# Optimization experiments

Hardware: AMD Instinct MI355X
Metric: run time of the kernel (lower is better)

The kernel has to match this reference:

```python
import jax, jax.numpy as jnp
import numpy as np

EPS = 1e-5  # torch BatchNorm2d default eps (eval mode with running stats)


def bn(x, g, b, m, v):
    # x: [B,C,H,W]; per-channel affine batchnorm in inference form
    return (x - m[:, None, None]) * (g[:, None, None] / jnp.sqrt(v[:, None, None] + EPS)) + b[:, None, None]


def self_attn(x, Wq, bq, Wk, bk, Wv, bv, rel_h, rel_w):
    # x: [B,C,H,W]; Wq/Wk/Wv: [C,C] (1x1 convs); rel_h: [C,H]; rel_w: [C,W]
    B, C, H, W = x.shape
    N = H * W
    q = jnp.einsum('oc,bchw->bohw', Wq, x).reshape(B, C, N) + bq[None, :, None]
    k = jnp.einsum('oc,bchw->bohw', Wk, x).reshape(B, C, N) + bk[None, :, None]
    v = jnp.einsum('oc,bchw->bohw', Wv, x).reshape(B, C, N) + bv[None, :, None]
    energy = jnp.einsum('bcn,bcm->bnm', q, k)                      # content: Q^T K
    pos = (rel_h[:, :, None] + rel_w[:, None, :]).reshape(C, N)    # [C, H*W]
    energy = energy + jnp.einsum('bcn,cm->bnm', q, pos)            # rel-pos bias term
    attn = jax.nn.softmax(energy, axis=-1)                         # [B,N,N]
    out = jnp.einsum('bcm,bnm->bcn', v, attn)                      # V @ attn^T
    return out.reshape(B, C, H, W)


def conv3x3(x, w):
    return jax.lax.conv_general_dilated(x, w, (1, 1), 'SAME',
                                        dimension_numbers=('NCHW', 'OIHW', 'NCHW'))


def setup_inputs() -> dict:
    key = jax.random.key(0)
    B, C, H, W, NH = 32, 512, 16, 16, 5
    ks = jax.random.split(key, 32)
    f = lambda i, shape, s=1.0: jax.random.normal(ks[i], shape, jnp.float32) * s
    inp = {
        'x0': f(0, (B, C, H, W)), 'x1': f(1, (B, C, H, W)), 'x2': f(2, (B, C, H, W)),
        'x3': f(3, (B, C, H, W)), 'x': f(4, (B, C, H, W)),
        'qW': f(5, (NH, C, C), 0.02), 'qB': f(6, (NH, C), 0.02),
        'kW': f(7, (NH, C, C), 0.02), 'kB': f(8, (NH, C), 0.02),
        'vW': f(9, (NH, C, C), 0.02), 'vB': f(10, (NH, C), 0.02),
        'relH': f(11, (NH, C, H)), 'relW': f(12, (NH, C, W)),
        'msw_W': f(13, (NH - 1, NH * C), 0.02),
        'msw_g': jnp.ones((NH - 1,)), 'msw_b': jnp.zeros((NH - 1,)),
        'msw_m': jnp.zeros((NH - 1,)), 'msw_v': jnp.ones((NH - 1,)),
        'fus_W': f(14, (C, C, 3, 3), 0.02),
        'fus_g': jnp.ones((C,)), 'fus_b': jnp.zeros((C,)),
        'fus_m': jnp.zeros((C,)), 'fus_v': jnp.ones((C,)),
        'top_g': jnp.ones((C,)), 'top_b': jnp.zeros((C,)),
        'top_m': jnp.zeros((C,)), 'top_v': jnp.ones((C,)),
        'h': 16, 'w': 16,
    }
    return inp


def reference(x0, x1, x2, x3, x, qW, qB, kW, kB, vW, vB, relH, relW,
              msw_W, msw_g, msw_b, msw_m, msw_v,
              fus_W, fus_g, fus_b, fus_m, fus_v,
              top_g, top_b, top_m, top_v, h, w):
    B, C, H, W = x.shape
    xs = jnp.stack([x0, x1, x2, x3, x])                            # [5,B,C,H,W]
    outs = jax.vmap(self_attn)(xs, qW, qB, kW, kB, vW, vB, relH, relW)  # [5,B,C,H,W]
    cat = outs.transpose(1, 0, 2, 3, 4).reshape(B, 5 * C, H, W)
    weights = jax.nn.sigmoid(bn(jnp.einsum('oc,bchw->bohw', msw_W, cat),
                                msw_g, msw_b, msw_m, msw_v))        # [B,4,H,W]
    x_ms = (weights[:, 0:1] * outs[0] + weights[:, 1:2] * outs[1]
            + weights[:, 2:3] * outs[2] + weights[:, 3:4] * outs[3] + outs[4])
    x_ms = jax.nn.relu(bn(conv3x3(x_ms, fus_W), fus_g, fus_b, fus_m, fus_v))
    out = jax.nn.relu(bn(x_ms + x, top_g, top_b, top_m, top_v))
    return out
```

## Files before the change

### kernel.cpp

```cpp
#include <hip/hip_runtime.h>
#include <cstdint>

using bf16x8  = __attribute__((ext_vector_type(8))) __bf16;
using f32x4   = __attribute__((ext_vector_type(4))) float;
using ushort8 = __attribute__((ext_vector_type(8))) unsigned short;

#define EPSN 1e-5f

__device__ __forceinline__ void gld16(const void* g, void* l) {
  __builtin_amdgcn_global_load_lds((const __attribute__((address_space(1))) void*)g,
                                   (__attribute__((address_space(3))) void*)l, 16, 0, 0);
}

__device__ __forceinline__ ushort f2bf(float f) {
  __bf16 h = (__bf16)f;
  return __builtin_bit_cast(unsigned short, h);
}
__device__ __forceinline__ float bf2f(ushort u) {
  union { uint32_t u; float f; } v; v.u = ((uint32_t)u) << 16; return v.f;
}

__global__ __launch_bounds__(256) void k_pre(const float* __restrict__ x0,
                                             const float* __restrict__ x1,
                                             const float* __restrict__ x2,
                                             const float* __restrict__ x3,
                                             const float* __restrict__ x4,
                                             const float* __restrict__ qW,
                                             const float* __restrict__ kW,
                                             const float* __restrict__ vW,
                                             const float* __restrict__ relH,
                                             const float* __restrict__ relW,
                                             const float* __restrict__ fg,
                                             const float* __restrict__ fb,
                                             const float* __restrict__ fm,
                                             const float* __restrict__ fv,
                                             const float* __restrict__ tg,
                                             const float* __restrict__ tb,
                                             const float* __restrict__ tm,
                                             const float* __restrict__ tv,
                                             ushort* __restrict__ xT,
                                             ushort* __restrict__ Wb,
                                             ushort* __restrict__ posb,
                                             float4* __restrict__ bnp) {
  __shared__ float tile[64][65];
  int bid = blockIdx.x;
  const int t = threadIdx.x;
  if (bid < 5120) {
    const int nt4 = bid & 3;  bid >>= 2;
    const int ct  = bid & 7;  bid >>= 3;
    const int b   = bid & 31; bid >>= 5;
    const int ix  = bid;
    const float* xs = ix == 0 ? x0 : ix == 1 ? x1 : ix == 2 ? x2 : ix == 3 ? x3 : x4;
    const float* src = xs + ((size_t)b * 512 + ct * 64) * 256 + nt4 * 64;
    const int col4 = (t & 15) * 4, r0 = t >> 4;
#pragma unroll
    for (int p = 0; p < 4; ++p) {
      int row = p * 16 + r0;
      float4 v = *(const float4*)(src + (size_t)row * 256 + col4);
      tile[row][col4 + 0] = v.x; tile[row][col4 + 1] = v.y;
      tile[row][col4 + 2] = v.z; tile[row][col4 + 3] = v.w;
    }
    __syncthreads();
    ushort* dst = xT + ((size_t)(ix * 32 + b) * 256 + nt4 * 64) * 512 + ct * 64;
    const int c8 = (t & 7) * 8, n0 = t >> 3;
#pragma unroll
    for (int p = 0; p < 2; ++p) {
      int nrow = p * 32 + n0;
      ushort8 o;
#pragma unroll
      for (int e = 0; e < 8; ++e) o[e] = f2bf(tile[c8 + e][nrow]);
      *(ushort8*)(dst + (size_t)nrow * 512 + c8) = o;
    }
  } else if (bid < 8960) {
    int idx = (bid - 5120) * 256 + t;
    int gi = idx * 4;
    int sel = gi / 1310720;
    int off = gi - sel * 1310720;
    const float* src = sel == 0 ? qW : (sel == 1 ? kW : vW);
    float4 vv = *(const float4*)(src + off);
    int h = off / 262144, rest = off - h * 262144;
    ushort4 o;
    o.x = f2bf(vv.x); o.y = f2bf(vv.y); o.z = f2bf(vv.z); o.w = f2bf(vv.w);
    *(ushort4*)(Wb + (size_t)(h * 3 + sel) * 262144 + rest) = o;
  } else if (bid < 9280) {
    int idx8 = (bid - 8960) * 256 + t;
    int e0 = idx8 * 8;
    int c0 = e0 & 511, m = (e0 >> 9) & 255, h = e0 >> 17;
    ushort8 o;
#pragma unroll
    for (int e = 0; e < 8; ++e) {
      int c = c0 + e;
      o[e] = f2bf(relH[((size_t)h * 512 + c) * 16 + (m >> 4)] +
                  relW[((size_t)h * 512 + c) * 16 + (m & 15)]);
    }
    *(ushort8*)(posb + e0) = o;
  } else {
    int o = (bid - 9280) * 256 + t;
    float sf = fg[o] * rsqrtf(fv[o] + EPSN);
    float c1 = fb[o] - fm[o] * sf;
    float st = tg[o] * rsqrtf(tv[o] + EPSN);
    float c2 = tb[o] - tm[o] * st;
    bnp[o] = make_float4(sf, c1, st, c2);
  }
}

__global__ __launch_bounds__(512, 4) void k_qkv3(const ushort* __restrict__ Wb,
                                                 const ushort* __restrict__ xT,
                                                 const ushort* __restrict__ posb,
                                                 const float* __restrict__ qB,
                                                 const float* __restrict__ kB,
                                                 const float* __restrict__ vB,
                                                 ushort* __restrict__ qT,
                                                 ushort* __restrict__ kpT,
                                                 ushort* __restrict__ vv) {
  extern __shared__ ushort ls[];
  const int t = threadIdx.x, lane = t & 63;
  const int w = t >> 6, wm = w >> 2, wn = w & 3, g = lane >> 4, l = lane & 15;
  int bid = blockIdx.x;
  bid = (bid & 7) * 240 + (bid >> 3);
  const int h = bid / 384;
  const int r = bid % 384;

  const ushort* Ag;
  const ushort* Bg;
  const bool partA = r < 256;
  int pt = 0, nt = 0, mt = 0, ntv = 0;
  if (partA) {
    pt = r >> 2; nt = r & 3;
    Ag = xT + ((size_t)h * 8192 + pt * 128) * 512;
    Bg = Wb + ((size_t)(h * 3 + (nt >> 1)) * 512 + (nt & 1) * 256) * 512;
  } else {
    const int r2 = r - 256;
    mt = r2 >> 5; ntv = r2 & 31;
    Ag = Wb + ((size_t)(h * 3 + 2) * 512 + mt * 128) * 512;
    Bg = xT + ((size_t)h * 8192 + ntv * 256) * 512;
  }

  f32x4 acc[4][4];
#pragma unroll
  for (int i = 0; i < 4; ++i)
#pragma unroll
    for (int j = 0; j < 4; ++j) acc[i][j] = f32x4{0.f, 0.f, 0.f, 0.f};

#define QKV_STAGE(tt, slot)                                                    \
  {                                                                            \
    const int kb_ = (tt) * 32;                                                 \
    ushort* sa_ = ls + (slot) * 4096;                                          \
    ushort* sb_ = ls + 12288 + (slot) * 8192;                                  \
    {                                                                          \
      int q_ = t;                                                              \
      int row_ = q_ >> 2, s4_ = q_ & 3;                                        \
      int src_ = s4_ ^ ((row_ ^ (row_ >> 2)) & 3);                             \
      gld16(Ag + (size_t)row_ * 512 + kb_ + src_ * 8, sa_ + q_ * 8);           \
    }                                                                          \
    _Pragma("unroll")                                                          \
    for (int p_ = 0; p_ < 2; ++p_) {                                           \
      int q_ = p_ * 512 + t;                                                   \
      int row_ = q_ >> 2, s4_ = q_ & 3;                                        \
      int src_ = s4_ ^ ((row_ ^ (row_ >> 2)) & 3);                             \
      gld16(Bg + (size_t)row_ * 512 + kb_ + src_ * 8, sb_ + q_ * 8);           \
    }                                                                          \
  }

#define QKV_COMPUTE(slot)                                                      \
  {                                                                            \
    ushort* sa_ = ls + (slot) * 4096;                                          \
    ushort* sb_ = ls + 12288 + (slot) * 8192;                                  \
    bf16x8 af[4], bfv[4];                                                      \
    _Pragma("unroll")                                                          \
    for (int j_ = 0; j_ < 4; ++j_) {                                           \
      int rb_ = wn * 64 + j_ * 16 + l;                                         \
      int sb2_ = g ^ ((rb_ ^ (rb_ >> 2)) & 3);                                 \
      bfv[j_] = *(const bf16x8*)(sb_ + rb_ * 32 + sb2_ * 8);                   \
    }                                                                          \
    _Pragma("unroll")                                                          \
    for (int i_ = 0; i_ < 4; ++i_) {                                           \
      int ra_ = wm * 64 + i_ * 16 + l;                                         \
      int sa2_ = g ^ ((ra_ ^ (ra_ >> 2)) & 3);                                 \
      af[i_] = *(const bf16x8*)(sa_ + ra_ * 32 + sa2_ * 8);                    \
    }                                                                          \
    asm volatile("s_waitcnt lgkmcnt(0)" ::: "memory");                         \
    __builtin_amdgcn_sched_barrier(0);                                         \
    __builtin_amdgcn_s_setprio(1);                                             \
    _Pragma("unroll")                                                          \
    for (int i_ = 0; i_ < 4; ++i_)                                             \
      _Pragma("unroll")                                                        \
      for (int j_ = 0; j_ < 4; ++j_)                                           \
        acc[i_][j_] = __builtin_amdgcn_mfma_f32_16x16x32_bf16(af[i_], bfv[j_], \
                                                              acc[i_][j_], 0, 0, 0); \
    __builtin_amdgcn_s_setprio(0);                                             \
  }

  QKV_STAGE(0, 0);
  QKV_STAGE(1, 1);
  for (int tt = 0; tt < 16; ++tt) {
    __builtin_amdgcn_s_barrier();
    if (tt < 14) { QKV_STAGE(tt + 2, (tt + 2) % 3); }
    __builtin_amdgcn_sched_barrier(0);
    if (tt < 14)       asm volatile("s_waitcnt vmcnt(6)" ::: "memory");
    else if (tt == 14) asm volatile("s_waitcnt vmcnt(3)" ::: "memory");
    else               asm volatile("s_waitcnt vmcnt(0)" ::: "memory");
    __builtin_amdgcn_s_barrier();
    __builtin_amdgcn_sched_barrier(0);
    QKV_COMPUTE(tt % 3);
  }
  __syncthreads();

  ushort(*Cs)[260] = (ushort(*)[260])ls;
  if (partA) {
    const bool isq = nt < 2;
    const float* bias = (isq ? qB : kB) + (size_t)h * 512 + (nt & 1) * 256;
    ushort* dst = isq ? qT : kpT;
    float bj[4];
#pragma unroll
    for (int j = 0; j < 4; ++j) bj[j] = bias[wn * 64 + j * 16 + l];
#pragma unroll
    for (int R = 0; R < 2; ++R) {
      if (wm == R) {
#pragma unroll
        for (int i = 0; i < 4; ++i)
#pragma unroll
          for (int j = 0; j < 4; ++j)
#pragma unroll
            for (int rr = 0; rr < 4; ++rr)
              Cs[i * 16 + g * 4 + rr][wn * 64 + j * 16 + l] = f2bf(acc[i][j][rr] + bj[j]);
      }
      __syncthreads();
#pragma unroll
      for (int it = 0; it < 4; ++it) {
        int lin = it * 512 + t;
        int row = lin >> 5, cc8 = (lin & 31) * 8;
        int pglob = pt * 128 + R * 64 + row;
        ushort8 cv = *(const ushort8*)&Cs[row][cc8];
        if (!isq) {
          ushort8 pv = *(const ushort8*)(posb + ((size_t)h * 256 + (pglob & 255)) * 512 +
                                         (nt & 1) * 256 + cc8);
#pragma unroll
          for (int e = 0; e < 8; ++e) cv[e] = f2bf(bf2f(cv[e]) + bf2f(pv[e]));
        }
        *(ushort8*)(dst + ((size_t)h * 8192 + pglob) * 512 + (nt & 1) * 256 + cc8) = cv;
      }
      if (R == 0) __syncthreads();
    }
  } else {
    const float* bias = vB + (size_t)h * 512 + mt * 128;
#pragma unroll
    for (int R = 0; R < 2; ++R) {
      if (wm == R) {
#pragma unroll
        for (int i = 0; i < 4; ++i) {
          float4 b4 = *(const float4*)(bias + R * 64 + i * 16 + g * 4);
#pragma unroll
          for (int j = 0; j < 4; ++j)
#pragma unroll
            for (int rr = 0; rr < 4; ++rr)
              Cs[i * 16 + g * 4 + rr][wn * 64 + j * 16 + l] =
                  f2bf(acc[i][j][rr] + ((const float*)&b4)[rr]);
        }
      }
      __syncthreads();
#pragma unroll
      for (int it = 0; it < 4; ++it) {
        int lin = it * 512 + t;
        int row = lin >> 5, cc8 = (lin & 31) * 8;
        int og = mt * 128 + R * 64 + row;
        ushort8 cv = *(const ushort8*)&Cs[row][cc8];
        *(ushort8*)(vv + (((size_t)(h * 32 + ntv)) * 512 + og) * 256 + cc8) = cv;
      }
      if (R == 0) __syncthreads();
    }
  }
#undef QKV_STAGE
#undef QKV_COMPUTE
}

__global__ __launch_bounds__(256) void k_attn(const ushort* __restrict__ qT,
                                              const ushort* __restrict__ kpT,
                                              const float* __restrict__ fusW,
                                              ushort* __restrict__ attn,
                                              ushort* __restrict__ Wconv) {
  __shared__ ushort sm[20480];
  __shared__ float red[4][64];
  __shared__ float comb[64];
  int bid = blockIdx.x;
  const int t = threadIdx.x;
  if (bid >= 640) {
    int p = (bid - 640) * 256 + t;
    const float* src = fusW + (size_t)p * 9;
    float vv[9];
#pragma unroll
    for (int s = 0; s < 9; ++s) vv[s] = src[s];
#pragma unroll
    for (int s = 0; s < 9; ++s) Wconv[(size_t)s * 262144 + p] = f2bf(vv[s]);
    return;
  }
  bid = (bid & 7) * 80 + (bid >> 3);
  const int rt = bid & 3;
  const int hb = bid >> 2;
  ushort* As = sm;
  ushort* Bs = sm + 4096;
  const ushort* Ag = qT + ((size_t)hb * 256 + rt * 64) * 512;
  const ushort* Bg = kpT + (size_t)hb * 256 * 512;
  const int lane = t & 63, w = t >> 6, g = lane >> 4, l = lane & 15;

  f32x4 acc[4][4];
#pragma unroll
  for (int i = 0; i < 4; ++i)
#pragma unroll
    for (int j = 0; j < 4; ++j) acc[i][j] = f32x4{0.f, 0.f, 0.f, 0.f};

  for (int kt = 0; kt < 8; ++kt) {
    const int kbase = kt * 64;
#pragma unroll
    for (int p = 0; p < 2; ++p) {
      int q = p * 256 + t;
      int row = q >> 3, slot = q & 7, srcs = slot ^ (row & 7);
      gld16(Ag + (size_t)row * 512 + kbase + srcs * 8, As + (p * 256 + w * 64) * 8);
    }
#pragma unroll
    for (int p = 0; p < 8; ++p) {
      int q = p * 256 + t;
      int row = q >> 3, slot = q & 7, srcs = slot ^ (row & 7);
      gld16(Bg + (size_t)row * 512 + kbase + srcs * 8, Bs + (p * 256 + w * 64) * 8);
    }
    __syncthreads();
#pragma unroll
    for (int kk = 0; kk < 2; ++kk) {
      bf16x8 af[4], bfv[4];
#pragma unroll
      for (int i = 0; i < 4; ++i) {
        int ra = i * 16 + l;
        int sa = (kk * 4 + g) ^ (ra & 7);
        af[i] = *(const bf16x8*)(As + ra * 64 + sa * 8);
        int rb = w * 64 + i * 16 + l;
        int sb = (kk * 4 + g) ^ (rb & 7);
        bfv[i] = *(const bf16x8*)(Bs + rb * 64 + sb * 8);
      }
#pragma unroll
      for (int i = 0; i < 4; ++i)
#pragma unroll
        for (int j = 0; j < 4; ++j)
          acc[i][j] = __builtin_amdgcn_mfma_f32_16x16x32_bf16(af[i], bfv[j], acc[i][j], 0, 0, 0);
    }
    __syncthreads();
  }

#pragma unroll
  for (int i = 0; i < 4; ++i)
#pragma unroll
    for (int rr = 0; rr < 4; ++rr) {
      float v = fmaxf(fmaxf(acc[i][0][rr], acc[i][1][rr]), fmaxf(acc[i][2][rr], acc[i][3][rr]));
#pragma unroll
      for (int m = 1; m < 16; m <<= 1) v = fmaxf(v, __shfl_xor(v, m));
      if (l == 0) red[w][i * 16 + g * 4 + rr] = v;
    }
  __syncthreads();
  if (t < 64) comb[t] = fmaxf(fmaxf(red[0][t], red[1][t]), fmaxf(red[2][t], red[3][t]));
  __syncthreads();
#pragma unroll
  for (int i = 0; i < 4; ++i)
#pragma unroll
    for (int rr = 0; rr < 4; ++rr) {
      float mx = comb[i * 16 + g * 4 + rr];
      float s = 0.f;
#pragma unroll
      for (int j = 0; j < 4; ++j) {
        float e = expf(acc[i][j][rr] - mx);
        acc[i][j][rr] = e;
        s += e;
      }
#pragma unroll
      for (int m = 1; m < 16; m <<= 1) s += __shfl_xor(s, m);
      if (l == 0) red[w][i * 16 + g * 4 + rr] = s;
    }
  __syncthreads();
  if (t < 64) comb[t] = red[0][t] + red[1][t] + red[2][t] + red[3][t];
  __syncthreads();
  ushort(*P)[260] = (ushort(*)[260])sm;
#pragma unroll
  for (int i = 0; i < 4; ++i)
#pragma unroll
    for (int rr = 0; rr < 4; ++rr) {
      int row = i * 16 + g * 4 + rr;
      float inv = 1.f / comb[row];
#pragma unroll
      for (int j = 0; j < 4; ++j)
        P[row][w * 64 + j * 16 + l] = f2bf(acc[i][j][rr] * inv);
    }
  __syncthreads();
  ushort* Arow = attn + (size_t)hb * 65536 + (size_t)rt * 16384;
#pragma unroll
  for (int it = 0; it < 8; ++it) {
    int lin = it * 256 + t;
    int row = lin >> 5, c8 = (lin & 31) * 8;
    ushort8 cv = *(const ushort8*)&P[row][c8];
    *(ushort8*)(Arow + (size_t)row * 256 + c8) = cv;
  }
}

__global__ __launch_bounds__(256, 4) void k_pv(const ushort* __restrict__ attn,
                                               const ushort* __restrict__ vv,
                                               ushort* __restrict__ OT) {
  __shared__ ushort pls[24576];
  const int t = threadIdx.x, lane = t & 63, w = t >> 6;
  const int wr = w >> 1, wc = w & 1, g = lane >> 4, l = lane & 15;
  int bid = blockIdx.x;
  bid = (bid & 7) * 160 + (bid >> 3);
  const int nt = bid & 3; bid >>= 2;
  const int mt = bid & 1; bid >>= 1;
  const size_t hb = (size_t)bid;
  const ushort* Ag = attn + (hb * 256 + mt * 128) * 256;
  const ushort* Bg = vv + (hb * 512 + nt * 128) * 256;

  f32x4 acc[4][4];
#pragma unroll
  for (int i = 0; i < 4; ++i)
#pragma unroll
    for (int j = 0; j < 4; ++j) acc[i][j] = f32x4{0.f, 0.f, 0.f, 0.f};

#define PV_STAGE(tt, slot)                                                     \
  {                                                                            \
    const int kb_ = (tt) * 32;                                                 \
    ushort* sa_ = pls + (slot) * 4096;                                         \
    ushort* sb_ = pls + 12288 + (slot) * 4096;                                 \
    _Pragma("unroll")                                                          \
    for (int p_ = 0; p_ < 2; ++p_) {                                           \
      int q_ = p_ * 256 + t;                                                   \
      int row_ = q_ >> 2, s4_ = q_ & 3;                                        \
      int src_ = s4_ ^ ((row_ ^ (row_ >> 2)) & 3);                             \
      gld16(Ag + (size_t)row_ * 256 + kb_ + src_ * 8, sa_ + q_ * 8);           \
      gld16(Bg + (size_t)row_ * 256 + kb_ + src_ * 8, sb_ + q_ * 8);           \
    }                                                                          \
  }

#define PV_COMPUTE(slot)                                                       \
  {                                                                            \
    ushort* sa_ = pls + (slot) * 4096;                                         \
    ushort* sb_ = pls + 12288 + (slot) * 4096;                                 \
    bf16x8 af[4], bfv[4];                                                      \
    _Pragma("unroll")                                                          \
    for (int i_ = 0; i_ < 4; ++i_) {                                           \
      int ra_ = wr * 64 + i_ * 16 + l;                                         \
      int sa2_ = g ^ ((ra_ ^ (ra_ >> 2)) & 3);                                 \
      af[i_] = *(const bf16x8*)(sa_ + ra_ * 32 + sa2_ * 8);                    \
      int rb_ = wc * 64 + i_ * 16 + l;                                         \
      int sb2_ = g ^ ((rb_ ^ (rb_ >> 2)) & 3);                                 \
      bfv[i_] = *(const bf16x8*)(sb_ + rb_ * 32 + sb2_ * 8);                   \
    }                                                                          \
    asm volatile("s_waitcnt lgkmcnt(0)" ::: "memory");                         \
    __builtin_amdgcn_sched_barrier(0);                                         \
    __builtin_amdgcn_s_setprio(1);                                             \
    _Pragma("unroll")                                                          \
    for (int i_ = 0; i_ < 4; ++i_)                                             \
      _Pragma("unroll")                                                        \
      for (int j_ = 0; j_ < 4; ++j_)                                           \
        acc[i_][j_] = __builtin_amdgcn_mfma_f32_16x16x32_bf16(af[i_], bfv[j_], \
                                                              acc[i_][j_], 0, 0, 0); \
    __builtin_amdgcn_s_setprio(0);                                             \
  }

  PV_STAGE(0, 0);
  PV_STAGE(1, 1);
  for (int tt = 0; tt < 8; ++tt) {
    __builtin_amdgcn_s_barrier();
    if (tt < 6) { PV_STAGE(tt + 2, (tt + 2) % 3); }
    __builtin_amdgcn_sched_barrier(0);
    if (tt < 6)       asm volatile("s_waitcnt vmcnt(8)" ::: "memory");
    else if (tt == 6) asm volatile("s_waitcnt vmcnt(4)" ::: "memory");
    else              asm volatile("s_waitcnt vmcnt(0)" ::: "memory");
    __builtin_amdgcn_s_barrier();
    __builtin_amdgcn_sched_barrier(0);
    PV_COMPUTE(tt % 3);
  }
  __syncthreads();

  ushort(*Cs)[148] = (ushort(*)[148])pls;
#pragma unroll
  for (int i = 0; i < 4; ++i)
#pragma unroll
    for (int j = 0; j < 4; ++j)
#pragma unroll
      for (int rr = 0; rr < 4; ++rr)
        Cs[wr * 64 + i * 16 + g * 4 + rr][wc * 64 + j * 16 + l] = f2bf(acc[i][j][rr]);
  __syncthreads();
#pragma unroll
  for (int it = 0; it < 8; ++it) {
    int lin = it * 256 + t;
    int row = lin >> 4, cc = (lin & 15) * 8;
    ushort8 cv = *(const ushort8*)&Cs[row][cc];
    *(ushort8*)(OT + (hb * 256 + mt * 128 + row) * 512 + nt * 128 + cc) = cv;
  }
#undef PV_STAGE
#undef PV_COMPUTE
}

__global__ __launch_bounds__(256) void k_weights(const ushort* __restrict__ OT,
                                                 const float* __restrict__ mswW,
                                                 const float* __restrict__ mg,
                                                 const float* __restrict__ mb,
                                                 const float* __restrict__ mm,
                                                 const float* __restrict__ mv,
                                                 ushort* __restrict__ xmsT) {
  __shared__ float msw[10240];
  const int t = threadIdx.x, lane = t & 63, w = t >> 6;
#pragma unroll
  for (int it = 0; it < 10; ++it) {
    int idx = it * 1024 + t * 4;
    *(float4*)(msw + idx) = *(const float4*)(mswW + idx);
  }
  __syncthreads();
  const size_t pix = (size_t)blockIdx.x * 4 + w;
  float o[5][2][4];
#pragma unroll
  for (int h = 0; h < 5; ++h)
#pragma unroll
    for (int hf = 0; hf < 2; ++hf) {
      ushort4 v = *(const ushort4*)(OT + ((size_t)h * 8192 + pix) * 512 + hf * 256 + lane * 4);
      o[h][hf][0] = bf2f(v.x); o[h][hf][1] = bf2f(v.y);
      o[h][hf][2] = bf2f(v.z); o[h][hf][3] = bf2f(v.w);
    }
  float a[4] = {0.f, 0.f, 0.f, 0.f};
#pragma unroll
  for (int j = 0; j < 4; ++j)
#pragma unroll
    for (int h = 0; h < 5; ++h)
#pragma unroll
      for (int hf = 0; hf < 2; ++hf) {
        float4 m4 = *(const float4*)(msw + j * 2560 + h * 512 + hf * 256 + lane * 4);
        a[j] += m4.x * o[h][hf][0] + m4.y * o[h][hf][1] +
                m4.z * o[h][hf][2] + m4.w * o[h][hf][3];
      }
#pragma unroll
  for (int m = 1; m < 64; m <<= 1) {
    a[0] += __shfl_xor(a[0], m); a[1] += __shfl_xor(a[1], m);
    a[2] += __shfl_xor(a[2], m); a[3] += __shfl_xor(a[3], m);
  }
  float wj[4];
#pragma unroll
  for (int j = 0; j < 4; ++j) {
    float val = (a[j] - mm[j]) * (mg[j] * rsqrtf(mv[j] + EPSN)) + mb[j];
    wj[j] = 1.f / (1.f + expf(-val));
  }
#pragma unroll
  for (int hf = 0; hf < 2; ++hf) {
    float r0 = wj[0] * o[0][hf][0] + wj[1] * o[1][hf][0] + wj[2] * o[2][hf][0] + wj[3] * o[3][hf][0] + o[4][hf][0];
    float r1 = wj[0] * o[0][hf][1] + wj[1] * o[1][hf][1] + wj[2] * o[2][hf][1] + wj[3] * o[3][hf][1] + o[4][hf][1];
    float r2 = wj[0] * o[0][hf][2] + wj[1] * o[1][hf][2] + wj[2] * o[2][hf][2] + wj[3] * o[3][hf][2] + o[4][hf][2];
    float r3 = wj[0] * o[0][hf][3] + wj[1] * o[1][hf][3] + wj[2] * o[2][hf][3] + wj[3] * o[3][hf][3] + o[4][hf][3];
    ushort4 pk; pk.x = f2bf(r0); pk.y = f2bf(r1); pk.z = f2bf(r2); pk.w = f2bf(r3);
    *(ushort4*)(xmsT + pix * 512 + hf * 256 + lane * 4) = pk;
  }
}

__global__ __launch_bounds__(256) void k_conv(const ushort* __restrict__ Wconv,
                                              const ushort* __restrict__ xmsT,
                                              const float* __restrict__ x,
                                              const float4* __restrict__ bnp,
                                              float* __restrict__ out) {
  __shared__ ushort As3[3 * 4096];
  __shared__ ushort xp[180 * 76];
  int bid = blockIdx.x;
  bid = (bid & 7) * 64 + (bid >> 3);
  const int ntl = bid & 1; bid >>= 1;
  const int mt = bid & 7;  bid >>= 3;
  const int bb = bid;
  const int y0 = ntl * 8;
  const int t = threadIdx.x, lane = t & 63;
  const int w = t >> 6, wm = w >> 1, wn = w & 1, g = lane >> 4, l = lane & 15;
  f32x4 acc[2][4];
#pragma unroll
  for (int i = 0; i < 2; ++i)
#pragma unroll
    for (int j = 0; j < 4; ++j) acc[i][j] = f32x4{0.f, 0.f, 0.f, 0.f};

  for (int cb = 0; cb < 8; ++cb) {
    __syncthreads();
    for (int u = t; u < 1440; u += 256) {
      int slot = u & 7;
      int xpi = (u >> 3) % 18;
      int rl = u / 144;
      int yg = y0 - 1 + rl, xg = xpi - 1;
      uint4 val = make_uint4(0, 0, 0, 0);
      if (yg >= 0 && yg < 16 && (unsigned)xg < 16u)
        val = *(const uint4*)(xmsT + ((size_t)bb * 256 + yg * 16 + xg) * 512 + cb * 64 + slot * 8);
      *(uint4*)(xp + (rl * 18 + xpi) * 76 + slot * 8) = val;
    }
    for (int dy = 0; dy < 3; ++dy) {
#pragma unroll
      for (int dx = 0; dx < 3; ++dx)
#pragma unroll
        for (int p = 0; p < 2; ++p) {
          int q = p * 256 + t;
          int row = q >> 3, slot = q & 7, srcs = slot ^ (row & 7);
          gld16(Wconv + ((size_t)(dy * 3 + dx) * 512 + mt * 64 + row) * 512 + cb * 64 + srcs * 8,
                As3 + dx * 4096 + q * 8);
        }
      __syncthreads();
#pragma unroll
      for (int dx = 0; dx < 3; ++dx)
#pragma unroll
        for (int kk = 0; kk < 2; ++kk) {
          bf16x8 af[2], bfv[4];
#pragma unroll
          for (int j = 0; j < 4; ++j) {
            int nl = wn * 64 + j * 16 + l;
            int pp = ((nl >> 4) + dy) * 18 + (nl & 15) + dx;
            bfv[j] = *(const bf16x8*)(xp + pp * 76 + (kk * 4 + g) * 8);
          }
#pragma unroll
          for (int i = 0; i < 2; ++i) {
            int ra = wm * 32 + i * 16 + l;
            int sa = (kk * 4 + g) ^ (ra & 7);
            af[i] = *(const bf16x8*)(As3 + dx * 4096 + ra * 64 + sa * 8);
          }
#pragma unroll
          for (int i = 0; i < 2; ++i)
#pragma unroll
            for (int j = 0; j < 4; ++j)
              acc[i][j] = __builtin_amdgcn_mfma_f32_16x16x32_bf16(af[i], bfv[j], acc[i][j], 0, 0, 0);
        }
      __syncthreads();
    }
  }
  const int o0 = mt * 64 + wm * 32;
#pragma unroll
  for (int i = 0; i < 2; ++i)
#pragma unroll
    for (int rr = 0; rr < 4; ++rr) {
      int o = o0 + i * 16 + g * 4 + rr;
      float4 p4 = bnp[o];
#pragma unroll
      for (int j = 0; j < 4; ++j) {
        int n = ntl * 128 + wn * 64 + j * 16 + l;
        size_t idx = ((size_t)bb * 512 + o) * 256 + n;
        float z = fmaxf(acc[i][j][rr] * p4.x + p4.y, 0.f);
        out[idx] = fmaxf((z + x[idx]) * p4.z + p4.w, 0.f);
      }
    }
}

extern "C" void kernel_launch(void* const* d_in, const int* in_sizes, int n_in,
                              void* d_out, int out_size, void* d_ws, size_t ws_size,
                              hipStream_t stream) {
  const float* x0   = (const float*)d_in[0];
  const float* x1   = (const float*)d_in[1];
  const float* x2   = (const float*)d_in[2];
  const float* x3   = (const float*)d_in[3];
  const float* x4   = (const float*)d_in[4];
  const float* qW   = (const float*)d_in[5];
  const float* qB   = (const float*)d_in[6];
  const float* kW   = (const float*)d_in[7];
  const float* kB   = (const float*)d_in[8];
  const float* vW   = (const float*)d_in[9];
  const float* vB   = (const float*)d_in[10];
  const float* relH = (const float*)d_in[11];
  const float* relW = (const float*)d_in[12];
  const float* mswW = (const float*)d_in[13];
  const float* msg  = (const float*)d_in[14];
  const float* msb  = (const float*)d_in[15];
  const float* msm  = (const float*)d_in[16];
  const float* msv  = (const float*)d_in[17];
  const float* fusW = (const float*)d_in[18];
  const float* fg   = (const float*)d_in[19];
  const float* fb   = (const float*)d_in[20];
  const float* fm   = (const float*)d_in[21];
  const float* fv   = (const float*)d_in[22];
  const float* tg   = (const float*)d_in[23];
  const float* tb   = (const float*)d_in[24];
  const float* tm   = (const float*)d_in[25];
  const float* tv   = (const float*)d_in[26];

  if (ws_size < 180355072ull) return;
  char* ws = (char*)d_ws;
  ushort* xT    = (ushort*)(ws + 0);
  ushort* attn  = (ushort*)(ws + 0);
  ushort* Wconv = (ushort*)(ws + 20971520);
  ushort* qT    = (ushort*)(ws + 41943040);
  ushort* xmsT  = (ushort*)(ws + 41943040);
  ushort* kpT   = (ushort*)(ws + 83886080);
  ushort* OT    = (ushort*)(ws + 83886080);
  ushort* vv    = (ushort*)(ws + 125829120);
  ushort* Wb    = (ushort*)(ws + 167772160);
  ushort* posb  = (ushort*)(ws + 175636480);
  float4* bnp   = (float4*)(ws + 176947200);

  hipFuncSetAttribute((const void*)k_qkv3,
                      hipFuncAttributeMaxDynamicSharedMemorySize, 73728);

  k_pre    <<<9282, 256, 0, stream>>>(x0, x1, x2, x3, x4, qW, kW, vW, relH, relW,
                                      fg, fb, fm, fv, tg, tb, tm, tv,
                                      xT, Wb, posb, (float4*)bnp);
  k_qkv3   <<<1920, 512, 73728, stream>>>(Wb, xT, posb, qB, kB, vB, qT, kpT, vv);
  k_attn   <<<1664, 256, 0, stream>>>(qT, kpT, fusW, attn, Wconv);
  k_pv     <<<1280, 256, 0, stream>>>(attn, vv, OT);
  k_weights<<<2048, 256, 0, stream>>>(OT, mswW, msg, msb, msm, msv, xmsT);
  k_conv   <<<512,  256, 0, stream>>>(Wconv, xmsT, x4, bnp, (float*)d_out);
}
```

Measured before the change: 246.4 us.

## Triple-buffer attention QK GEMM loads and batch four pixels per weights wave

The QK^T stage of the attention kernel now uses a three-slot LDS ring with a K-step of 32. Loads for two future tiles stay in flight while MFMAs run on the current one, with explicit vmcnt waits, raw barriers and setprio around the MFMA block. A new XOR swizzle keeps LDS reads free of bank conflicts. Separately, the mixing-weights kernel now handles four pixels per wave, so each 40KB msw weight copy into LDS is amortized over 16 pixels and the grid drops to 512 blocks. This trades more LDS use and hand-tuned wait counts (fragile if load counts change) for better load/compute overlap.

Result: slower. 275.1 us (+11.7%).

```diff
diff --git a/kernel.cpp b/kernel.cpp
--- a/kernel.cpp
+++ b/kernel.cpp
@@ -279,7 +279,7 @@
                                               const float* __restrict__ fusW,
                                               ushort* __restrict__ attn,
                                               ushort* __restrict__ Wconv) {
-  __shared__ ushort sm[20480];
+  __shared__ ushort sm[30720];
   __shared__ float red[4][64];
   __shared__ float comb[64];
   int bid = blockIdx.x;
@@ -297,8 +297,6 @@
   bid = (bid & 7) * 80 + (bid >> 3);
   const int rt = bid & 3;
   const int hb = bid >> 2;
-  ushort* As = sm;
-  ushort* Bs = sm + 4096;
   const ushort* Ag = qT + ((size_t)hb * 256 + rt * 64) * 512;
   const ushort* Bg = kpT + (size_t)hb * 256 * 512;
   const int lane = t & 63, w = t >> 6, g = lane >> 4, l = lane & 15;
@@ -309,41 +307,70 @@
 #pragma unroll
     for (int j = 0; j < 4; ++j) acc[i][j] = f32x4{0.f, 0.f, 0.f, 0.f};
 
-  for (int kt = 0; kt < 8; ++kt) {
-    const int kbase = kt * 64;
-#pragma unroll
-    for (int p = 0; p < 2; ++p) {
-      int q = p * 256 + t;
-      int row = q >> 3, slot = q & 7, srcs = slot ^ (row & 7);
-      gld16(Ag + (size_t)row * 512 + kbase + srcs * 8, As + (p * 256 + w * 64) * 8);
-    }
-#pragma unroll
-    for (int p = 0; p < 8; ++p) {
-      int q = p * 256 + t;
-      int row = q >> 3, slot = q & 7, srcs = slot ^ (row & 7);
-      gld16(Bg + (size_t)row * 512 + kbase + srcs * 8, Bs + (p * 256 + w * 64) * 8);
-    }
-    __syncthreads();
-#pragma unroll
-    for (int kk = 0; kk < 2; ++kk) {
-      bf16x8 af[4], bfv[4];
-#pragma unroll
-      for (int i = 0; i < 4; ++i) {
-        int ra = i * 16 + l;
-        int sa = (kk * 4 + g) ^ (ra & 7);
-        af[i] = *(const bf16x8*)(As + ra * 64 + sa * 8);
-        int rb = w * 64 + i * 16 + l;
-        int sb = (kk * 4 + g) ^ (rb & 7);
-        bfv[i] = *(const bf16x8*)(Bs + rb * 64 + sb * 8);
-      }
-#pragma unroll
-      for (int i = 0; i < 4; ++i)
-#pragma unroll
-        for (int j = 0; j < 4; ++j)
-          acc[i][j] = __builtin_amdgcn_mfma_f32_16x16x32_bf16(af[i], bfv[j], acc[i][j], 0, 0, 0);
-    }
-    __syncthreads();
-  }
+#define AT_STAGE(tt, slot)                                                     \
+  {                                                                            \
+    const int kb_ = (tt) * 32;                                                 \
+    ushort* sa_ = sm + (slot) * 2048;                                          \
+    ushort* sb_ = sm + 6144 + (slot) * 8192;                                   \
+    {                                                                          \
+      int q_ = t;                                                              \
+      int row_ = q_ >> 2, s4_ = q_ & 3;                                        \
+      int src_ = s4_ ^ ((row_ ^ (row_ >> 2)) & 3);                             \
+      gld16(Ag + (size_t)row_ * 512 + kb_ + src_ * 8, sa_ + q_ * 8);           \
+    }                                                                          \
+    _Pragma("unroll")                                                          \
+    for (int p_ = 0; p_ < 4; ++p_) {                                           \
+      int q_ = p_ * 256 + t;                                                   \
+      int row_ = q_ >> 2, s4_ = q_ & 3;                                        \
+      int src_ = s4_ ^ ((row_ ^ (row_ >> 2)) & 3);                             \
+      gld16(Bg + (size_t)row_ * 512 + kb_ + src_ * 8, sb_ + q_ * 8);           \
+    }                                                                          \
+  }
+
+#define AT_COMPUTE(slot)                                                       \
+  {                                                                            \
+    ushort* sa_ = sm + (slot) * 2048;                                          \
+    ushort* sb_ = sm + 6144 + (slot) * 8192;                                   \
+    bf16x8 af[4], bfv[4];                                                      \
+    _Pragma("unroll")                                                          \
+    for (int j_ = 0; j_ < 4; ++j_) {                                           \
+      int rb_ = w * 64 + j_ * 16 + l;                                          \
+      int sb2_ = g ^ ((rb_ ^ (rb_ >> 2)) & 3);                                 \
+      bfv[j_] = *(const bf16x8*)(sb_ + rb_ * 32 + sb2_ * 8);                   \
+    }                                                                          \
+    _Pragma("unroll")                                                          \
+    for (int i_ = 0; i_ < 4; ++i_) {                                           \
+      int ra_ = i_ * 16 + l;                                                   \
+      int sa2_ = g ^ ((ra_ ^ (ra_ >> 2)) & 3);                                 \
+      af[i_] = *(const bf16x8*)(sa_ + ra_ * 32 + sa2_ * 8);                    \
+    }                                                                          \
+    asm volatile("s_waitcnt lgkmcnt(0)" ::: "memory");                         \
+    __builtin_amdgcn_sched_barrier(0);                                         \
+    __builtin_amdgcn_s_setprio(1);                                             \
+    _Pragma("unroll")                                                          \
+    for (int i_ = 0; i_ < 4; ++i_)                                             \
+      _Pragma("unroll")                                                        \
+      for (int j_ = 0; j_ < 4; ++j_)                                           \
+        acc[i_][j_] = __builtin_amdgcn_mfma_f32_16x16x32_bf16(af[i_], bfv[j_], \
+                                                              acc[i_][j_], 0, 0, 0); \
+    __builtin_amdgcn_s_setprio(0);                                             \
+  }
+
+  AT_STAGE(0, 0);
+  AT_STAGE(1, 1);
+  for (int tt = 0; tt < 16; ++tt) {
+    __builtin_amdgcn_s_barrier();
+    if (tt < 14) { AT_STAGE(tt + 2, (tt + 2) % 3); }
+    __builtin_amdgcn_sched_barrier(0);
+    if (tt < 14)       asm volatile("s_waitcnt vmcnt(10)" ::: "memory");
+    else if (tt == 14) asm volatile("s_waitcnt vmcnt(5)" ::: "memory");
+    else               asm volatile("s_waitcnt vmcnt(0)" ::: "memory");
+    __builtin_amdgcn_s_barrier();
+    __builtin_amdgcn_sched_barrier(0);
+    AT_COMPUTE(tt % 3);
+  }
+#undef AT_STAGE
+#undef AT_COMPUTE
 
 #pragma unroll
   for (int i = 0; i < 4; ++i)
@@ -509,46 +536,55 @@
     *(float4*)(msw + idx) = *(const float4*)(mswW + idx);
   }
   __syncthreads();
-  const size_t pix = (size_t)blockIdx.x * 4 + w;
-  float o[5][2][4];
-#pragma unroll
-  for (int h = 0; h < 5; ++h)
+  float bnc[4][2];
+#pragma unroll
+  for (int j = 0; j < 4; ++j) {
+    bnc[j][0] = mg[j] * rsqrtf(mv[j] + EPSN);
+    bnc[j][1] = mb[j] - mm[j] * bnc[j][0];
+  }
+#pragma unroll
+  for (int p = 0; p < 4; ++p) {
+    const size_t pix = (size_t)blockIdx.x * 16 + w * 4 + p;
+    float o[5][2][4];
+#pragma unroll
+    for (int h = 0; h < 5; ++h)
+#pragma unroll
+      for (int hf = 0; hf < 2; ++hf) {
+        ushort4 v = *(const ushort4*)(OT + ((size_t)h * 8192 + pix) * 512 + hf * 256 + lane * 4);
+        o[h][hf][0] = bf2f(v.x); o[h][hf][1] = bf2f(v.y);
+        o[h][hf][2] = bf2f(v.z); o[h][hf][3] = bf2f(v.w);
+      }
+    float a[4] = {0.f, 0.f, 0.f, 0.f};
+#pragma unroll
+    for (int j = 0; j < 4; ++j)
+#pragma unroll
+      for (int h = 0; h < 5; ++h)
+#pragma unroll
+        for (int hf = 0; hf < 2; ++hf) {
+          float4 m4 = *(const float4*)(msw + j * 2560 + h * 512 + hf * 256 + lane * 4);
+          a[j] += m4.x * o[h][hf][0] + m4.y * o[h][hf][1] +
+                  m4.z * o[h][hf][2] + m4.w * o[h][hf][3];
+        }
+#pragma unroll
+    for (int m = 1; m < 64; m <<= 1) {
+      a[0] += __shfl_xor(a[0], m); a[1] += __shfl_xor(a[1], m);
+      a[2] += __shfl_xor(a[2], m); a[3] += __shfl_xor(a[3], m);
+    }
+    float wj[4];
+#pragma unroll
+    for (int j = 0; j < 4; ++j) {
+      float val = a[j] * bnc[j][0] + bnc[j][1];
+      wj[j] = 1.f / (1.f + expf(-val));
+    }
 #pragma unroll
     for (int hf = 0; hf < 2; ++hf) {
-      ushort4 v = *(const ushort4*)(OT + ((size_t)h * 8192 + pix) * 512 + hf * 256 + lane * 4);
-      o[h][hf][0] = bf2f(v.x); o[h][hf][1] = bf2f(v.y);
-      o[h][hf][2] = bf2f(v.z); o[h][hf][3] = bf2f(v.w);
-    }
-  float a[4] = {0.f, 0.f, 0.f, 0.f};
-#pragma unroll
-  for (int j = 0; j < 4; ++j)
-#pragma unroll
-    for (int h = 0; h < 5; ++h)
-#pragma unroll
-      for (int hf = 0; hf < 2; ++hf) {
-        float4 m4 = *(const float4*)(msw + j * 2560 + h * 512 + hf * 256 + lane * 4);
-        a[j] += m4.x * o[h][hf][0] + m4.y * o[h][hf][1] +
-                m4.z * o[h][hf][2] + m4.w * o[h][hf][3];
-      }
-#pragma unroll
-  for (int m = 1; m < 64; m <<= 1) {
-    a[0] += __shfl_xor(a[0], m); a[1] += __shfl_xor(a[1], m);
-    a[2] += __shfl_xor(a[2], m); a[3] += __shfl_xor(a[3], m);
-  }
-  float wj[4];
-#pragma unroll
-  for (int j = 0; j < 4; ++j) {
-    float val = (a[j] - mm[j]) * (mg[j] * rsqrtf(mv[j] + EPSN)) + mb[j];
-    wj[j] = 1.f / (1.f + expf(-val));
-  }
-#pragma unroll
-  for (int hf = 0; hf < 2; ++hf) {
-    float r0 = wj[0] * o[0][hf][0] + wj[1] * o[1][hf][0] + wj[2] * o[2][hf][0] + wj[3] * o[3][hf][0] + o[4][hf][0];
-    float r1 = wj[0] * o[0][hf][1] + wj[1] * o[1][hf][1] + wj[2] * o[2][hf][1] + wj[3] * o[3][hf][1] + o[4][hf][1];
-    float r2 = wj[0] * o[0][hf][2] + wj[1] * o[1][hf][2] + wj[2] * o[2][hf][2] + wj[3] * o[3][hf][2] + o[4][hf][2];
-    float r3 = wj[0] * o[0][hf][3] + wj[1] * o[1][hf][3] + wj[2] * o[2][hf][3] + wj[3] * o[3][hf][3] + o[4][hf][3];
-    ushort4 pk; pk.x = f2bf(r0); pk.y = f2bf(r1); pk.z = f2bf(r2); pk.w = f2bf(r3);
-    *(ushort4*)(xmsT + pix * 512 + hf * 256 + lane * 4) = pk;
+      float r0 = wj[0] * o[0][hf][0] + wj[1] * o[1][hf][0] + wj[2] * o[2][hf][0] + wj[3] * o[3][hf][0] + o[4][hf][0];
+      float r1 = wj[0] * o[0][hf][1] + wj[1] * o[1][hf][1] + wj[2] * o[2][hf][1] + wj[3] * o[3][hf][1] + o[4][hf][1];
+      float r2 = wj[0] * o[0][hf][2] + wj[1] * o[1][hf][2] + wj[2] * o[2][hf][2] + wj[3] * o[3][hf][2] + o[4][hf][2];
+      float r3 = wj[0] * o[0][hf][3] + wj[1] * o[1][hf][3] + wj[2] * o[2][hf][3] + wj[3] * o[3][hf][3] + o[4][hf][3];
+      ushort4 pk; pk.x = f2bf(r0); pk.y = f2bf(r1); pk.z = f2bf(r2); pk.w = f2bf(r3);
+      *(ushort4*)(xmsT + pix * 512 + hf * 256 + lane * 4) = pk;
+    }
   }
 }
 
@@ -693,6 +729,6 @@
   k_qkv3   <<<1920, 512, 73728, stream>>>(Wb, xT, posb, qB, kB, vB, qT, kpT, vv);
   k_attn   <<<1664, 256, 0, stream>>>(qT, kpT, fusW, attn, Wconv);
   k_pv     <<<1280, 256, 0, stream>>>(attn, vv, OT);
-  k_weights<<<2048, 256, 0, stream>>>(OT, mswW, msg, msb, msm, msv, xmsT);
+  k_weights<<<512,  256, 0, stream>>>(OT, mswW, msg, msb, msm, msv, xmsT);
   k_conv   <<<512,  256, 0, stream>>>(Wconv, xmsT, x4, bnp, (float*)d_out);
 }
```

## Halve conv output-channel tile and load all nine tap weights per k-block

Applied to the files above, without the earlier changes.

The 3x3 conv kernel now computes 32 output channels per block instead of 64, doubling the grid to 1024 blocks. All nine filter taps for a 64-channel slice are loaded into shared memory in one shot, which removes the per-dy barriers. Each wave now covers 32 pixels with all 32 channels. The aim is more blocks in flight and fewer synchronisations on a grid that was too small for the GPU. The cost is that each block does less reuse, so the input halo tile gets reloaded twice as often across the grid, and shared memory per block changes.

Result: slower. 261.8 us (+6.3%).

```diff
diff --git a/kernel.cpp b/kernel.cpp
--- a/kernel.cpp
+++ b/kernel.cpp
@@ -557,21 +557,21 @@
                                               const float* __restrict__ x,
                                               const float4* __restrict__ bnp,
                                               float* __restrict__ out) {
-  __shared__ ushort As3[3 * 4096];
+  __shared__ ushort As9[9 * 2048];
   __shared__ ushort xp[180 * 76];
   int bid = blockIdx.x;
-  bid = (bid & 7) * 64 + (bid >> 3);
-  const int ntl = bid & 1; bid >>= 1;
-  const int mt = bid & 7;  bid >>= 3;
-  const int bb = bid;
+  bid = (bid & 7) * 128 + (bid >> 3);
+  const int ntl = bid & 1;  bid >>= 1;
+  const int mt  = bid & 15; bid >>= 4;
+  const int bb  = bid;
   const int y0 = ntl * 8;
   const int t = threadIdx.x, lane = t & 63;
-  const int w = t >> 6, wm = w >> 1, wn = w & 1, g = lane >> 4, l = lane & 15;
-  f32x4 acc[2][4];
+  const int w = t >> 6, g = lane >> 4, l = lane & 15;
+  f32x4 acc[2][2];
 #pragma unroll
   for (int i = 0; i < 2; ++i)
 #pragma unroll
-    for (int j = 0; j < 4; ++j) acc[i][j] = f32x4{0.f, 0.f, 0.f, 0.f};
+    for (int j = 0; j < 2; ++j) acc[i][j] = f32x4{0.f, 0.f, 0.f, 0.f};
 
   for (int cb = 0; cb < 8; ++cb) {
     __syncthreads();
@@ -585,44 +585,40 @@
         val = *(const uint4*)(xmsT + ((size_t)bb * 256 + yg * 16 + xg) * 512 + cb * 64 + slot * 8);
       *(uint4*)(xp + (rl * 18 + xpi) * 76 + slot * 8) = val;
     }
-    for (int dy = 0; dy < 3; ++dy) {
+    {
+      int row = t >> 3, slot = t & 7, srcs = slot ^ (row & 7);
+#pragma unroll
+      for (int s = 0; s < 9; ++s)
+        gld16(Wconv + ((size_t)s * 512 + mt * 32 + row) * 512 + cb * 64 + srcs * 8,
+              As9 + s * 2048 + t * 8);
+    }
+    __syncthreads();
+    for (int dy = 0; dy < 3; ++dy)
 #pragma unroll
       for (int dx = 0; dx < 3; ++dx)
 #pragma unroll
-        for (int p = 0; p < 2; ++p) {
-          int q = p * 256 + t;
-          int row = q >> 3, slot = q & 7, srcs = slot ^ (row & 7);
-          gld16(Wconv + ((size_t)(dy * 3 + dx) * 512 + mt * 64 + row) * 512 + cb * 64 + srcs * 8,
-                As3 + dx * 4096 + q * 8);
-        }
-      __syncthreads();
-#pragma unroll
-      for (int dx = 0; dx < 3; ++dx)
-#pragma unroll
         for (int kk = 0; kk < 2; ++kk) {
-          bf16x8 af[2], bfv[4];
-#pragma unroll
-          for (int j = 0; j < 4; ++j) {
-            int nl = wn * 64 + j * 16 + l;
+          bf16x8 af[2], bfv[2];
+#pragma unroll
+          for (int j = 0; j < 2; ++j) {
+            int nl = w * 32 + j * 16 + l;
             int pp = ((nl >> 4) + dy) * 18 + (nl & 15) + dx;
             bfv[j] = *(const bf16x8*)(xp + pp * 76 + (kk * 4 + g) * 8);
           }
 #pragma unroll
           for (int i = 0; i < 2; ++i) {
-            int ra = wm * 32 + i * 16 + l;
+            int ra = i * 16 + l;
             int sa = (kk * 4 + g) ^ (ra & 7);
-            af[i] = *(const bf16x8*)(As3 + dx * 4096 + ra * 64 + sa * 8);
+            af[i] = *(const bf16x8*)(As9 + (dy * 3 + dx) * 2048 + ra * 64 + sa * 8);
           }
 #pragma unroll
           for (int i = 0; i < 2; ++i)
 #pragma unroll
-            for (int j = 0; j < 4; ++j)
+            for (int j = 0; j < 2; ++j)
               acc[i][j] = __builtin_amdgcn_mfma_f32_16x16x32_bf16(af[i], bfv[j], acc[i][j], 0, 0, 0);
         }
-      __syncthreads();
-    }
-  }
-  const int o0 = mt * 64 + wm * 32;
+  }
+  const int o0 = mt * 32;
 #pragma unroll
   for (int i = 0; i < 2; ++i)
 #pragma unroll
@@ -630,8 +626,8 @@
       int o = o0 + i * 16 + g * 4 + rr;
       float4 p4 = bnp[o];
 #pragma unroll
-      for (int j = 0; j < 4; ++j) {
-        int n = ntl * 128 + wn * 64 + j * 16 + l;
+      for (int j = 0; j < 2; ++j) {
+        int n = ntl * 128 + w * 32 + j * 16 + l;
         size_t idx = ((size_t)bb * 512 + o) * 256 + n;
         float z = fmaxf(acc[i][j][rr] * p4.x + p4.y, 0.f);
         out[idx] = fmaxf((z + x[idx]) * p4.z + p4.w, 0.f);
@@ -694,5 +690,5 @@
   k_attn   <<<1664, 256, 0, stream>>>(qT, kpT, fusW, attn, Wconv);
   k_pv     <<<1280, 256, 0, stream>>>(attn, vv, OT);
   k_weights<<<2048, 256, 0, stream>>>(OT, mswW, msg, msb, msm, msv, xmsT);
-  k_conv   <<<512,  256, 0, stream>>>(Wconv, xmsT, x4, bnp, (float*)d_out);
-}
+  k_conv   <<<1024, 256, 0, stream>>>(Wconv, xmsT, x4, bnp, (float*)d_out);
+}
```
